# Kernel optimization log

Hardware: AMD Instinct MI355X
Metric: run time of the kernel (lower is better)

## Reference

```python
import jax, jax.numpy as jnp
import numpy as np

B, N, T = 256, 512, 96
E, H, K = 8, 128, 2
PROB_THRESHOLD = 0.05
# SG auto-anneal: first forward sets temperature = t_max = 10.0 (cosine decay at step 0)
TEMP = 10.0


def setup_inputs() -> dict:
    key = jax.random.key(0)
    ks = jax.random.split(key, 8)
    s_g = 1.0 / np.sqrt(T)
    s_1 = 1.0 / np.sqrt(T)
    s_2 = 1.0 / np.sqrt(H)
    return {
        "x": jax.random.normal(ks[0], (B, N, T), dtype=jnp.float32),
        "Wg": jax.random.uniform(ks[1], (E, T), jnp.float32, -s_g, s_g),   # gate Linear(T, E)
        "bg": jax.random.uniform(ks[2], (E,), jnp.float32, -s_g, s_g),
        "W1": jax.random.uniform(ks[3], (E, T, H), jnp.float32, -s_1, s_1),  # stacked MLPExpert fc1
        "b1": jax.random.uniform(ks[4], (E, H), jnp.float32, -s_1, s_1),
        "W2": jax.random.uniform(ks[5], (E, H, T), jnp.float32, -s_2, s_2),  # stacked MLPExpert fc2
        "b2": jax.random.uniform(ks[6], (E, T), jnp.float32, -s_2, s_2),
        "route_scale": jnp.asarray(1.2, dtype=jnp.float32),
    }


def reference(x, Wg, bg, W1, b1, W2, b2, route_scale):
    b, n, t = x.shape
    BN = b * n
    xf = x.reshape(BN, t)                              # [BN, T]

    # ---- SG gate (eval mode: no noise; temp = t_max after first anneal step) ----
    logits = (xf @ Wg.T + bg) / TEMP                   # [BN, E]
    probs = jax.nn.softmax(logits, axis=-1)
    topw, topi = jax.lax.top_k(probs, K)               # [BN, K]
    w = topw / (jnp.sum(topw, axis=-1, keepdims=True) + 1e-12)  # topk_weights_norm

    # ---- SEA routing: capacity generous (never binds for this config); topk indices
    # are distinct so duplicate-expert reroute never triggers. Route is valid iff
    # normalized prob >= prob_threshold; invalid routes are passthrough (copy x). ----
    mask = w >= PROB_THRESHOLD                         # compute_mask [BN, K]

    # ---- SEE experts (MLPExpert with residual), computed densely per expert ----
    h = jax.nn.relu(jnp.einsum('bt,eth->ebh', xf, W1) + b1[:, None, :])   # [E, BN, H]
    y_all = jnp.einsum('ebh,eht->ebt', h, W2) + b2[:, None, :] + xf[None] # [E, BN, T]

    # gather each token's chosen expert outputs
    y_sel = y_all[topi, jnp.arange(BN)[:, None]]       # [BN, K, T]
    contrib = jnp.where(mask[..., None], y_sel, xf[:, None, :])

    # ---- weighted combine (SEE normalizes again, then scales) ----
    wn = w / jnp.clip(jnp.sum(w, axis=-1, keepdims=True), 1e-12)
    mixed = jnp.sum(contrib * wn[..., None], axis=1) * route_scale        # [BN, T]

    util = jnp.sum(mask[..., None] * jax.nn.one_hot(topi, E, dtype=xf.dtype), axis=1)
    return mixed.reshape(b, n, t), util.reshape(b, n, E)
```

## Files before the change

kernel.cpp:

```cpp
#include <hip/hip_runtime.h>
#include <hip/hip_bf16.h>

#define BN_TOTAL   131072
#define T_DIM      96
#define E_NUM      8
#define H_DIM      128
#define CAP        131072
#define PTHRESH    0.05f
#define NBLK       64

typedef _Float16 f16x8 __attribute__((ext_vector_type(8)));
typedef _Float16 f16x4 __attribute__((ext_vector_type(4)));
typedef float    f32x4 __attribute__((ext_vector_type(4)));

#define OFF_TOK    1024
#define OFF_SCALE  (OFF_TOK   + E_NUM * CAP * 4)
#define OFF_MASK   (OFF_SCALE + E_NUM * CAP * 4)
#define OFF_COEF   (OFF_MASK  + BN_TOTAL * 4)
#define OFF_YBUF   (OFF_COEF  + BN_TOTAL * 4)
#define OFF_XH     (OFF_YBUF + 2 * BN_TOTAL * T_DIM * 2)
#define OFF_W1T    (OFF_XH   + BN_TOTAL * T_DIM * 2)
#define OFF_W2T    (OFF_W1T  + E_NUM * H_DIM * T_DIM * 2)
#define WS_NEED    ((size_t)OFF_YBUF + (size_t)2 * BN_TOTAL * T_DIM * 4)


__global__ void zero_cnt_kernel(int* __restrict__ cnt) {
    if (threadIdx.x < E_NUM) cnt[threadIdx.x] = 0;
}

__global__ __launch_bounds__(256) void prep_kernel(
    const float* __restrict__ W1, const float* __restrict__ W2,
    _Float16* __restrict__ w1T, _Float16* __restrict__ w2T)
{
    __shared__ _Float16 tile[128 * 136];
    const int tid = threadIdx.x;
    const bool isW1 = blockIdx.x < 8;
    const int e = blockIdx.x & 7;
    const int R = isW1 ? T_DIM : H_DIM;
    const int C = isW1 ? H_DIM : T_DIM;
    const int S = isW1 ? 104 : 136;
    const float* src = (isW1 ? W1 : W2) + (size_t)e * T_DIM * H_DIM;
    _Float16* dst = (isW1 ? w1T : w2T) + (size_t)e * T_DIM * H_DIM;

    const int nb = (R >> 2) * (C >> 2);
    for (int b = tid; b < nb; b += 256) {
        const int r4 = b / (C >> 2), c4 = b % (C >> 2);
#pragma unroll
        for (int i = 0; i < 4; ++i) {
            const float4 v = *reinterpret_cast<const float4*>(src + (size_t)(4 * r4 + i) * C + 4 * c4);
            tile[(4 * c4 + 0) * S + 4 * r4 + i] = (_Float16)v.x;
            tile[(4 * c4 + 1) * S + 4 * r4 + i] = (_Float16)v.y;
            tile[(4 * c4 + 2) * S + 4 * r4 + i] = (_Float16)v.z;
            tile[(4 * c4 + 3) * S + 4 * r4 + i] = (_Float16)v.w;
        }
    }
    __syncthreads();
    const int chunks = C * (R >> 3);
    for (int q = tid; q < chunks; q += 256) {
        const int cr = q / (R >> 3), k = q % (R >> 3);
        *reinterpret_cast<f16x8*>(dst + (size_t)cr * R + 8 * k) =
            *reinterpret_cast<const f16x8*>(&tile[cr * S + 8 * k]);
    }
}

template<bool GATHER>
__global__ __launch_bounds__(1024) void gate_kernel(
    const float* __restrict__ x, const float* __restrict__ Wg,
    const float* __restrict__ bg, const float* __restrict__ rs_p,
    float* __restrict__ mixed, float* __restrict__ util,
    int* __restrict__ cnt, int* __restrict__ toklist, float* __restrict__ scalelist,
    int* __restrict__ maskbuf, float* __restrict__ coefbuf, _Float16* __restrict__ xh)
{
    __shared__ float wg_s[E_NUM][T_DIM];
    __shared__ float bg_s[E_NUM];
    __shared__ int wcnt[16][E_NUM];
    __shared__ int wbase[16][E_NUM];

    const int tid = threadIdx.x;
    for (int i = tid; i < E_NUM * T_DIM; i += 1024) wg_s[i / T_DIM][i % T_DIM] = Wg[i];
    if (tid < E_NUM) bg_s[tid] = bg[tid];
    __syncthreads();

    const int g   = tid >> 2;
    const int sub = tid & 3;
    const int token = blockIdx.x * 256 + g;
    const float* xr_f = x + (size_t)token * T_DIM + sub * 24;

    float4 xv[6];
#pragma unroll
    for (int i = 0; i < 6; ++i) xv[i] = reinterpret_cast<const float4*>(xr_f)[i];

    float logit[E_NUM];
#pragma unroll
    for (int e = 0; e < E_NUM; ++e) logit[e] = 0.0f;
#pragma unroll
    for (int i = 0; i < 6; ++i) {
#pragma unroll
        for (int e = 0; e < E_NUM; ++e) {
            const float4 wv = *reinterpret_cast<const float4*>(&wg_s[e][sub * 24 + 4 * i]);
            logit[e] = fmaf(xv[i].x, wv.x, logit[e]);
            logit[e] = fmaf(xv[i].y, wv.y, logit[e]);
            logit[e] = fmaf(xv[i].z, wv.z, logit[e]);
            logit[e] = fmaf(xv[i].w, wv.w, logit[e]);
        }
    }
#pragma unroll
    for (int e = 0; e < E_NUM; ++e) {
        logit[e] += __shfl_xor(logit[e], 1);
        logit[e] += __shfl_xor(logit[e], 2);
        logit[e] = (logit[e] + bg_s[e]) / 10.0f;
    }

    float mx = logit[0];
#pragma unroll
    for (int e = 1; e < E_NUM; ++e) mx = fmaxf(mx, logit[e]);
    float p[E_NUM]; float s = 0.0f;
#pragma unroll
    for (int e = 0; e < E_NUM; ++e) { p[e] = __expf(logit[e] - mx); s += p[e]; }
    const float inv_s = 1.0f / s;
#pragma unroll
    for (int e = 0; e < E_NUM; ++e) p[e] *= inv_s;

    int i0 = 0; float p0 = p[0];
#pragma unroll
    for (int e = 1; e < E_NUM; ++e) { if (p[e] > p0) { p0 = p[e]; i0 = e; } }
    int i1 = -1; float p1 = -1.0f;
#pragma unroll
    for (int e = 0; e < E_NUM; ++e) { if (e != i0 && p[e] > p1) { p1 = p[e]; i1 = e; } }

    const float denom0 = p0 + p1 + 1e-12f;
    const float w0 = p0 / denom0, w1 = p1 / denom0;
    const bool m0 = (w0 >= PTHRESH), m1 = (w1 >= PTHRESH);
    const float sumw = w0 + w1;
    const float denom1 = fmaxf(sumw, 1e-12f);
    const float wn0 = w0 / denom1, wn1 = w1 / denom1;
    const float rs = *rs_p;
    const float coef = rs * (wn0 + wn1);
    const bool lead = (sub == 0);

    if (GATHER) {
        _Float16* xr = xh + (size_t)token * T_DIM + sub * 24;
#pragma unroll
        for (int i = 0; i < 6; ++i) {
            f16x4 h4;
            h4[0] = (_Float16)xv[i].x; h4[1] = (_Float16)xv[i].y;
            h4[2] = (_Float16)xv[i].z; h4[3] = (_Float16)xv[i].w;
            reinterpret_cast<f16x4*>(xr)[i] = h4;
        }
        if (lead) { coefbuf[token] = coef; maskbuf[token] = (m0 ? 1 : 0) | (m1 ? 2 : 0); }
    } else {
        float* mr = mixed + (size_t)token * T_DIM + sub * 24;
#pragma unroll
        for (int i = 0; i < 6; ++i)
            reinterpret_cast<float4*>(mr)[i] =
                make_float4(coef * xv[i].x, coef * xv[i].y, coef * xv[i].z, coef * xv[i].w);
    }

    if (lead) {
        float u[E_NUM];
#pragma unroll
        for (int e = 0; e < E_NUM; ++e)
            u[e] = (((e == i0) && m0) || ((e == i1) && m1)) ? 1.0f : 0.0f;
        float4* u4 = reinterpret_cast<float4*>(util + (size_t)token * E_NUM);
        u4[0] = make_float4(u[0], u[1], u[2], u[3]);
        u4[1] = make_float4(u[4], u[5], u[6], u[7]);
    }

    const int lane = tid & 63;
    const int wv_id = tid >> 6;
    const unsigned long long lt = (1ULL << lane) - 1ULL;

    int wcnt_mine = 0, offA = 0, offB = 0;
#pragma unroll
    for (int e = 0; e < E_NUM; ++e) {
        const unsigned long long A = __ballot(lead && m0 && (i0 == e));
        const unsigned long long B = __ballot(lead && m1 && (i1 == e));
        const int na = __popcll(A), nb = __popcll(B);
        if (lane == e) wcnt_mine = na + nb;
        if (lead && m0 && (i0 == e)) offA = __popcll(A & lt);
        if (lead && m1 && (i1 == e)) offB = na + __popcll(B & lt);
    }
    if (lane < E_NUM) wcnt[wv_id][lane] = wcnt_mine;
    __syncthreads();
    if (tid < E_NUM) {
        int c[16], tot = 0;
#pragma unroll
        for (int w = 0; w < 16; ++w) { c[w] = wcnt[w][tid]; tot += c[w]; }
        int run = atomicAdd(&cnt[tid], tot);
#pragma unroll
        for (int w = 0; w < 16; ++w) { wbase[w][tid] = run; run += c[w]; }
    }
    __syncthreads();

    if (lead && m0) {
        const int pos = wbase[wv_id][i0] + offA;
        toklist[i0 * CAP + pos] = (token << 1);
        scalelist[i0 * CAP + pos] = rs * wn0;
    }
    if (lead && m1) {
        const int pos = wbase[wv_id][i1] + offB;
        toklist[i1 * CAP + pos] = (token << 1) | 1;
        scalelist[i1 * CAP + pos] = rs * wn1;
    }
}

template<bool GATHER>
__global__ __launch_bounds__(256, 2) void expert_kernel(
    const float* __restrict__ x, const _Float16* __restrict__ xh,
    const float* __restrict__ W1, const float* __restrict__ b1,
    const float* __restrict__ W2, const float* __restrict__ b2,
    const _Float16* __restrict__ w1T, const _Float16* __restrict__ w2T,
    float* __restrict__ mixed, _Float16* __restrict__ ybh,
    const int* __restrict__ cnt, const int* __restrict__ toklist,
    const float* __restrict__ scalelist)
{
    __shared__ __align__(16) _Float16 Hs[2][64 * 136];

    const int e = blockIdx.y;
    const int count = cnt[e];
    if ((int)blockIdx.x * 64 >= count) return;

    const int tid  = threadIdx.x;
    const int w    = tid >> 6;
    const int lane = tid & 63;
    const int lm   = lane & 15;
    const int lg4  = lane >> 4;
    const int mhalf = w & 1;
    const int nhalf = w >> 1;

    const int*   tl = toklist   + (size_t)e * CAP;
    const float* sl = scalelist + (size_t)e * CAP;

    f16x8 w1f[3][4];
    {
        const _Float16* w1e = w1T + (size_t)e * H_DIM * T_DIM;
        const float*    gW1 = W1  + (size_t)e * T_DIM * H_DIM;
#pragma unroll
        for (int ks = 0; ks < 3; ++ks)
#pragma unroll
            for (int n = 0; n < 4; ++n) {
                const int h = nhalf * 64 + n * 16 + lm;
                if (GATHER) {
                    w1f[ks][n] = *reinterpret_cast<const f16x8*>(
                        w1e + (size_t)h * T_DIM + ks * 32 + lg4 * 8);
                } else {
                    f16x8 v;
#pragma unroll
                    for (int j = 0; j < 8; ++j)
                        v[j] = (_Float16)gW1[(size_t)(ks * 32 + lg4 * 8 + j) * H_DIM + h];
                    w1f[ks][n] = v;
                }
            }
    }
    f16x8 w2f[4][3];
    {
        const _Float16* w2e = w2T + (size_t)e * H_DIM * T_DIM;
        const float*    gW2 = W2  + (size_t)e * H_DIM * T_DIM;
#pragma unroll
        for (int ks = 0; ks < 4; ++ks)
#pragma unroll
            for (int n = 0; n < 3; ++n) {
                const int t = nhalf * 48 + n * 16 + lm;
                if (GATHER) {
                    w2f[ks][n] = *reinterpret_cast<const f16x8*>(
                        w2e + (size_t)t * H_DIM + ks * 32 + lg4 * 8);
                } else {
                    f16x8 v;
#pragma unroll
                    for (int j = 0; j < 8; ++j)
                        v[j] = (_Float16)gW2[(size_t)(ks * 32 + lg4 * 8 + j) * T_DIM + t];
                    w2f[ks][n] = v;
                }
            }
    }
    float4 b1v[4], b2v[3];
#pragma unroll
    for (int n = 0; n < 4; ++n)
        b1v[n] = *reinterpret_cast<const float4*>(b1 + e * H_DIM + nhalf * 64 + n * 16 + lg4 * 4);
#pragma unroll
    for (int n = 0; n < 3; ++n)
        b2v[n] = *reinterpret_cast<const float4*>(b2 + e * T_DIM + nhalf * 48 + n * 16 + lg4 * 4);

    int buf = 0;
    for (int t0 = blockIdx.x * 64; t0 < count; t0 += NBLK * 64) {
        const int nt = min(64, count - t0);

        int packedi[2]; float sci[2]; bool val[2]; int rowi[2];
#pragma unroll
        for (int mt = 0; mt < 2; ++mt) {
            const int slot = (mhalf * 2 + mt) * 16 + lm;
            val[mt] = slot < nt;
            const int gi = t0 + (val[mt] ? slot : 0);
            packedi[mt] = tl[gi];
            rowi[mt] = packedi[mt] >> 1;
            sci[mt] = sl[gi];
        }

        f16x8 xf[2][3];
#pragma unroll
        for (int mt = 0; mt < 2; ++mt)
#pragma unroll
            for (int ks = 0; ks < 3; ++ks) {
                if (GATHER) {
                    xf[mt][ks] = *reinterpret_cast<const f16x8*>(
                        xh + (size_t)rowi[mt] * T_DIM + ks * 32 + lg4 * 8);
                } else {
                    const float* xp = x + (size_t)rowi[mt] * T_DIM + ks * 32 + lg4 * 8;
                    f16x8 v;
#pragma unroll
                    for (int j = 0; j < 8; ++j) v[j] = (_Float16)xp[j];
                    xf[mt][ks] = v;
                }
            }

        f32x4 acc1[2][4];
#pragma unroll
        for (int mt = 0; mt < 2; ++mt)
#pragma unroll
            for (int n = 0; n < 4; ++n) acc1[mt][n] = f32x4{0.f, 0.f, 0.f, 0.f};
#pragma unroll
        for (int ks = 0; ks < 3; ++ks)
#pragma unroll
            for (int n = 0; n < 4; ++n) {
                acc1[0][n] = __builtin_amdgcn_mfma_f32_16x16x32_f16(w1f[ks][n], xf[0][ks], acc1[0][n], 0, 0, 0);
                acc1[1][n] = __builtin_amdgcn_mfma_f32_16x16x32_f16(w1f[ks][n], xf[1][ks], acc1[1][n], 0, 0, 0);
            }

#pragma unroll
        for (int mt = 0; mt < 2; ++mt) {
            const int tok = (mhalf * 2 + mt) * 16 + lm;
#pragma unroll
            for (int n = 0; n < 4; ++n) {
                const float* bb = reinterpret_cast<const float*>(&b1v[n]);
                f16x4 hv;
#pragma unroll
                for (int r = 0; r < 4; ++r)
                    hv[r] = (_Float16)fmaxf(acc1[mt][n][r] + bb[r], 0.0f);
                *reinterpret_cast<f16x4*>(&Hs[buf][tok * 136 + nhalf * 64 + n * 16 + lg4 * 4]) = hv;
            }
        }
        __syncthreads();

        f32x4 acc2[2][3];
#pragma unroll
        for (int mt = 0; mt < 2; ++mt)
#pragma unroll
            for (int n = 0; n < 3; ++n) acc2[mt][n] = f32x4{0.f, 0.f, 0.f, 0.f};
#pragma unroll
        for (int ks = 0; ks < 4; ++ks) {
            const f16x8 hf0 = *reinterpret_cast<const f16x8*>(
                &Hs[buf][((mhalf * 2 + 0) * 16 + lm) * 136 + ks * 32 + lg4 * 8]);
            const f16x8 hf1 = *reinterpret_cast<const f16x8*>(
                &Hs[buf][((mhalf * 2 + 1) * 16 + lm) * 136 + ks * 32 + lg4 * 8]);
#pragma unroll
            for (int n = 0; n < 3; ++n) {
                acc2[0][n] = __builtin_amdgcn_mfma_f32_16x16x32_f16(w2f[ks][n], hf0, acc2[0][n], 0, 0, 0);
                acc2[1][n] = __builtin_amdgcn_mfma_f32_16x16x32_f16(w2f[ks][n], hf1, acc2[1][n], 0, 0, 0);
            }
        }

#pragma unroll
        for (int mt = 0; mt < 2; ++mt) {
            if (val[mt]) {
#pragma unroll
                for (int n = 0; n < 3; ++n) {
                    const float* bb = reinterpret_cast<const float*>(&b2v[n]);
                    f16x4 yv;
#pragma unroll
                    for (int r = 0; r < 4; ++r)
                        yv[r] = (_Float16)(sci[mt] * (acc2[mt][n][r] + bb[r]));
                    if (GATHER) {
                        *reinterpret_cast<f16x4*>(
                            ybh + (size_t)packedi[mt] * T_DIM + nhalf * 48 + n * 16 + lg4 * 4) = yv;
                    } else {
#pragma unroll
                        for (int r = 0; r < 4; ++r)
                            atomicAdd(&mixed[(size_t)(packedi[mt] >> 1) * T_DIM +
                                             nhalf * 48 + n * 16 + lg4 * 4 + r], (float)yv[r]);
                    }
                }
            }
        }
        buf ^= 1;
    }
}

__global__ __launch_bounds__(256) void finalize_kernel(
    const _Float16* __restrict__ xh, const _Float16* __restrict__ ybh,
    const int* __restrict__ maskbuf, const float* __restrict__ coefbuf,
    float* __restrict__ mixed)
{
    const int tid = threadIdx.x;
    const int token = blockIdx.x * 32 + (tid >> 3);
    const int seg = (tid & 7) * 12;

    const float coef = coefbuf[token];
    const int mask = maskbuf[token];

    const f16x4* xs = reinterpret_cast<const f16x4*>(xh + (size_t)token * T_DIM + seg);
    float4* od = reinterpret_cast<float4*>(mixed + (size_t)token * T_DIM + seg);

    float4 r[3];
#pragma unroll
    for (int q = 0; q < 3; ++q) {
        const f16x4 xv = xs[q];
        r[q] = make_float4(coef * (float)xv[0], coef * (float)xv[1],
                           coef * (float)xv[2], coef * (float)xv[3]);
    }
    if (mask & 1) {
        const f16x4* ys = reinterpret_cast<const f16x4*>(ybh + (size_t)(2 * token) * T_DIM + seg);
#pragma unroll
        for (int q = 0; q < 3; ++q) {
            const f16x4 yv = ys[q];
            r[q].x += (float)yv[0]; r[q].y += (float)yv[1];
            r[q].z += (float)yv[2]; r[q].w += (float)yv[3];
        }
    }
    if (mask & 2) {
        const f16x4* ys = reinterpret_cast<const f16x4*>(ybh + (size_t)(2 * token + 1) * T_DIM + seg);
#pragma unroll
        for (int q = 0; q < 3; ++q) {
            const f16x4 yv = ys[q];
            r[q].x += (float)yv[0]; r[q].y += (float)yv[1];
            r[q].z += (float)yv[2]; r[q].w += (float)yv[3];
        }
    }
#pragma unroll
    for (int q = 0; q < 3; ++q) od[q] = r[q];
}

extern "C" void kernel_launch(void* const* d_in, const int* in_sizes, int n_in,
                              void* d_out, int out_size, void* d_ws, size_t ws_size,
                              hipStream_t stream)
{
    const float* x  = (const float*)d_in[0];
    const float* Wg = (const float*)d_in[1];
    const float* bg = (const float*)d_in[2];
    const float* W1 = (const float*)d_in[3];
    const float* b1 = (const float*)d_in[4];
    const float* W2 = (const float*)d_in[5];
    const float* b2 = (const float*)d_in[6];
    const float* rs = (const float*)d_in[7];

    float* mixed = (float*)d_out;
    float* util  = mixed + (size_t)BN_TOTAL * T_DIM;

    char* ws = (char*)d_ws;
    int*      cnt       = (int*)ws;
    int*      toklist   = (int*)(ws + OFF_TOK);
    float*    scalelist = (float*)(ws + OFF_SCALE);
    int*      maskbuf   = (int*)(ws + OFF_MASK);
    float*    coefbuf   = (float*)(ws + OFF_COEF);
    _Float16* ybh       = (_Float16*)(ws + OFF_YBUF);
    _Float16* xh        = (_Float16*)(ws + OFF_XH);
    _Float16* w1T       = (_Float16*)(ws + OFF_W1T);
    _Float16* w2T       = (_Float16*)(ws + OFF_W2T);

    const bool gather = (ws_size >= WS_NEED);

    zero_cnt_kernel<<<1, 64, 0, stream>>>(cnt);
    if (gather) {
        prep_kernel<<<16, 256, 0, stream>>>(W1, W2, w1T, w2T);
        gate_kernel<true><<<BN_TOTAL / 256, 1024, 0, stream>>>(
            x, Wg, bg, rs, mixed, util, cnt, toklist, scalelist, maskbuf, coefbuf, xh);
        expert_kernel<true><<<dim3(NBLK, E_NUM), 256, 0, stream>>>(
            x, xh, W1, b1, W2, b2, w1T, w2T, mixed, ybh, cnt, toklist, scalelist);
        finalize_kernel<<<BN_TOTAL / 32, 256, 0, stream>>>(
            xh, ybh, maskbuf, coefbuf, mixed);
    } else {
        gate_kernel<false><<<BN_TOTAL / 256, 1024, 0, stream>>>(
            x, Wg, bg, rs, mixed, util, cnt, toklist, scalelist, maskbuf, coefbuf, xh);
        expert_kernel<false><<<dim3(NBLK, E_NUM), 256, 0, stream>>>(
            x, xh, W1, b1, W2, b2, w1T, w2T, mixed, ybh, cnt, toklist, scalelist);
    }
}
```

Baseline: 93.80 us.

## Fuse finalize into expert kernel via grid barrier; fold counter zeroing into prep

Removes the separate finalize launch by adding a software grid-wide barrier at the end of the expert kernel, after which all 512 blocks run the finalize loop with a grid-stride pattern. The counter zeroing moves into the prep kernel, saving a second launch. The cost is a spin-wait barrier that only works if all 512 blocks are co-resident (256 CUs at 2 blocks each), plus removing the early exit so idle blocks still reach the barrier. This also makes each block's tail longer.

```diff
diff --git a/kernel.cpp b/kernel.cpp
--- a/kernel.cpp
+++ b/kernel.cpp
@@ -28,12 +28,28 @@
     if (threadIdx.x < E_NUM) cnt[threadIdx.x] = 0;
 }
 
+__device__ __forceinline__ void grid_barrier(int* bar, int target) {
+    __syncthreads();
+    if (threadIdx.x == 0) {
+        __threadfence();
+        atomicAdd(bar, 1);
+        while (__hip_atomic_load(bar, __ATOMIC_RELAXED, __HIP_MEMORY_SCOPE_AGENT) < target) {}
+        __threadfence();
+    }
+    __syncthreads();
+}
+
 __global__ __launch_bounds__(256) void prep_kernel(
     const float* __restrict__ W1, const float* __restrict__ W2,
-    _Float16* __restrict__ w1T, _Float16* __restrict__ w2T)
+    _Float16* __restrict__ w1T, _Float16* __restrict__ w2T,
+    int* __restrict__ cnt, int* __restrict__ bar)
 {
     __shared__ _Float16 tile[128 * 136];
     const int tid = threadIdx.x;
+    if (blockIdx.x == 0) {
+        if (tid < E_NUM) cnt[tid] = 0;
+        if (tid == E_NUM) *bar = 0;
+    }
     const bool isW1 = blockIdx.x < 8;
     const int e = blockIdx.x & 7;
     const int R = isW1 ? T_DIM : H_DIM;
@@ -212,13 +228,14 @@
     const _Float16* __restrict__ w1T, const _Float16* __restrict__ w2T,
     float* __restrict__ mixed, _Float16* __restrict__ ybh,
     const int* __restrict__ cnt, const int* __restrict__ toklist,
-    const float* __restrict__ scalelist)
+    const float* __restrict__ scalelist,
+    const int* __restrict__ maskbuf, const float* __restrict__ coefbuf,
+    int* __restrict__ bar)
 {
     __shared__ __align__(16) _Float16 Hs[2][64 * 136];
 
     const int e = blockIdx.y;
     const int count = cnt[e];
-    if ((int)blockIdx.x * 64 >= count) return;
 
     const int tid  = threadIdx.x;
     const int w    = tid >> 6;
@@ -383,50 +400,50 @@
         }
         buf ^= 1;
     }
-}
-
-__global__ __launch_bounds__(256) void finalize_kernel(
-    const _Float16* __restrict__ xh, const _Float16* __restrict__ ybh,
-    const int* __restrict__ maskbuf, const float* __restrict__ coefbuf,
-    float* __restrict__ mixed)
-{
-    const int tid = threadIdx.x;
-    const int token = blockIdx.x * 32 + (tid >> 3);
-    const int seg = (tid & 7) * 12;
-
-    const float coef = coefbuf[token];
-    const int mask = maskbuf[token];
-
-    const f16x4* xs = reinterpret_cast<const f16x4*>(xh + (size_t)token * T_DIM + seg);
-    float4* od = reinterpret_cast<float4*>(mixed + (size_t)token * T_DIM + seg);
-
-    float4 r[3];
-#pragma unroll
-    for (int q = 0; q < 3; ++q) {
-        const f16x4 xv = xs[q];
-        r[q] = make_float4(coef * (float)xv[0], coef * (float)xv[1],
-                           coef * (float)xv[2], coef * (float)xv[3]);
-    }
-    if (mask & 1) {
-        const f16x4* ys = reinterpret_cast<const f16x4*>(ybh + (size_t)(2 * token) * T_DIM + seg);
-#pragma unroll
-        for (int q = 0; q < 3; ++q) {
-            const f16x4 yv = ys[q];
-            r[q].x += (float)yv[0]; r[q].y += (float)yv[1];
-            r[q].z += (float)yv[2]; r[q].w += (float)yv[3];
-        }
-    }
-    if (mask & 2) {
-        const f16x4* ys = reinterpret_cast<const f16x4*>(ybh + (size_t)(2 * token + 1) * T_DIM + seg);
-#pragma unroll
-        for (int q = 0; q < 3; ++q) {
-            const f16x4 yv = ys[q];
-            r[q].x += (float)yv[0]; r[q].y += (float)yv[1];
-            r[q].z += (float)yv[2]; r[q].w += (float)yv[3];
-        }
-    }
-#pragma unroll
-    for (int q = 0; q < 3; ++q) od[q] = r[q];
+
+    if (GATHER) {
+        grid_barrier(bar, NBLK * E_NUM);
+
+        const int fid = blockIdx.y * NBLK + blockIdx.x;
+        for (int base = fid * 32; base < BN_TOTAL; base += NBLK * E_NUM * 32) {
+            const int token = base + (tid >> 3);
+            const int seg = (tid & 7) * 12;
+
+            const float coef = coefbuf[token];
+            const int mask = maskbuf[token];
+
+            const f16x4* xs = reinterpret_cast<const f16x4*>(xh + (size_t)token * T_DIM + seg);
+            float4* od = reinterpret_cast<float4*>(mixed + (size_t)token * T_DIM + seg);
+
+            float4 r[3];
+#pragma unroll
+            for (int q = 0; q < 3; ++q) {
+                const f16x4 xv = xs[q];
+                r[q] = make_float4(coef * (float)xv[0], coef * (float)xv[1],
+                                   coef * (float)xv[2], coef * (float)xv[3]);
+            }
+            if (mask & 1) {
+                const f16x4* ys = reinterpret_cast<const f16x4*>(ybh + (size_t)(2 * token) * T_DIM + seg);
+#pragma unroll
+                for (int q = 0; q < 3; ++q) {
+                    const f16x4 yv = ys[q];
+                    r[q].x += (float)yv[0]; r[q].y += (float)yv[1];
+                    r[q].z += (float)yv[2]; r[q].w += (float)yv[3];
+                }
+            }
+            if (mask & 2) {
+                const f16x4* ys = reinterpret_cast<const f16x4*>(ybh + (size_t)(2 * token + 1) * T_DIM + seg);
+#pragma unroll
+                for (int q = 0; q < 3; ++q) {
+                    const f16x4 yv = ys[q];
+                    r[q].x += (float)yv[0]; r[q].y += (float)yv[1];
+                    r[q].z += (float)yv[2]; r[q].w += (float)yv[3];
+                }
+            }
+#pragma unroll
+            for (int q = 0; q < 3; ++q) od[q] = r[q];
+        }
+    }
 }
 
 extern "C" void kernel_launch(void* const* d_in, const int* in_sizes, int n_in,
@@ -447,6 +464,7 @@
 
     char* ws = (char*)d_ws;
     int*      cnt       = (int*)ws;
+    int*      bar       = (int*)(ws + 64);
     int*      toklist   = (int*)(ws + OFF_TOK);
     float*    scalelist = (float*)(ws + OFF_SCALE);
     int*      maskbuf   = (int*)(ws + OFF_MASK);
@@ -458,19 +476,19 @@
 
     const bool gather = (ws_size >= WS_NEED);
 
-    zero_cnt_kernel<<<1, 64, 0, stream>>>(cnt);
     if (gather) {
-        prep_kernel<<<16, 256, 0, stream>>>(W1, W2, w1T, w2T);
+        prep_kernel<<<16, 256, 0, stream>>>(W1, W2, w1T, w2T, cnt, bar);
         gate_kernel<true><<<BN_TOTAL / 256, 1024, 0, stream>>>(
             x, Wg, bg, rs, mixed, util, cnt, toklist, scalelist, maskbuf, coefbuf, xh);
         expert_kernel<true><<<dim3(NBLK, E_NUM), 256, 0, stream>>>(
-            x, xh, W1, b1, W2, b2, w1T, w2T, mixed, ybh, cnt, toklist, scalelist);
-        finalize_kernel<<<BN_TOTAL / 32, 256, 0, stream>>>(
-            xh, ybh, maskbuf, coefbuf, mixed);
+            x, xh, W1, b1, W2, b2, w1T, w2T, mixed, ybh, cnt, toklist, scalelist,
+            maskbuf, coefbuf, bar);
     } else {
+        zero_cnt_kernel<<<1, 64, 0, stream>>>(cnt);
         gate_kernel<false><<<BN_TOTAL / 256, 1024, 0, stream>>>(
             x, Wg, bg, rs, mixed, util, cnt, toklist, scalelist, maskbuf, coefbuf, xh);
         expert_kernel<false><<<dim3(NBLK, E_NUM), 256, 0, stream>>>(
-            x, xh, W1, b1, W2, b2, w1T, w2T, mixed, ybh, cnt, toklist, scalelist);
-    }
-}
+            x, xh, W1, b1, W2, b2, w1T, w2T, mixed, ybh, cnt, toklist, scalelist,
+            maskbuf, coefbuf, bar);
+    }
+}
```

Result: slower. 157.9 us (+68.4%).
